# Performance work log

Measured on AMD Instinct MI355X. Metric: run time of the kernel, lower is better.

The kernel has to match this reference:

```python
import jax, jax.numpy as jnp
import numpy as np

B, S, D_MODEL, H = 2, 2048, 1024, 16
DEPTH = D_MODEL // H


def setup_inputs() -> dict:
    key = jax.random.key(0)
    ks = jax.random.split(key, 12)
    s = 1.0 / np.sqrt(D_MODEL)
    inp = {
        "q": jax.random.normal(ks[0], (B, S, D_MODEL), jnp.float32),
        "k": jax.random.normal(ks[1], (B, S, D_MODEL), jnp.float32),
        "v": jax.random.normal(ks[2], (B, S, D_MODEL), jnp.float32),
        # CTRL-style causal mask: 1 where position is disallowed (future), 0 otherwise
        "mask": jnp.triu(jnp.ones((S, S), jnp.float32), k=1),
        "Wq_w": jax.random.normal(ks[3], (D_MODEL, D_MODEL), jnp.float32) * s,
        "Wq_b": jax.random.normal(ks[4], (D_MODEL,), jnp.float32) * s,
        "Wk_w": jax.random.normal(ks[5], (D_MODEL, D_MODEL), jnp.float32) * s,
        "Wk_b": jax.random.normal(ks[6], (D_MODEL,), jnp.float32) * s,
        "Wv_w": jax.random.normal(ks[7], (D_MODEL, D_MODEL), jnp.float32) * s,
        "Wv_b": jax.random.normal(ks[8], (D_MODEL,), jnp.float32) * s,
        "dense_w": jax.random.normal(ks[9], (D_MODEL, D_MODEL), jnp.float32) * s,
        "dense_b": jax.random.normal(ks[10], (D_MODEL,), jnp.float32) * s,
    }
    return inp


def _split_heads(x):
    # [B, S, D] -> [B, H, S, depth]
    b, s, _ = x.shape
    return x.reshape(b, s, H, DEPTH).transpose(0, 2, 1, 3)


def reference(q, k, v, mask, Wq_w, Wq_b, Wk_w, Wk_b, Wv_w, Wv_b, dense_w, dense_b):
    b = q.shape[0]
    # torch Linear: y = x @ W^T + b
    qh = _split_heads(q @ Wq_w.T + Wq_b)  # [B,H,Sq,dh]
    kh = _split_heads(k @ Wk_w.T + Wk_b)  # [B,H,Sk,dh]
    vh = _split_heads(v @ Wv_w.T + Wv_b)  # [B,H,Sk,dh]

    scale = 1.0 / np.sqrt(DEPTH)
    logits = jnp.einsum("bhqd,bhkd->bhqk", qh, kh) * scale  # [B,H,Sq,Sk]
    nd, ns = logits.shape[-2], logits.shape[-1]
    logits = logits + mask[ns - nd:ns, :ns] * -10000.0
    attn = jax.nn.softmax(logits, axis=-1)
    ctx = jnp.einsum("bhqk,bhkd->bhqd", attn, vh)  # [B,H,Sq,dh]
    ctx = ctx.transpose(0, 2, 1, 3).reshape(b, -1, D_MODEL)  # [B,Sq,D]
    out = ctx @ dense_w.T + dense_b
    return out
```

## Files before the change

### kernel.cpp

```cpp
#include <hip/hip_runtime.h>
#include <hip/hip_bf16.h>

typedef __bf16 bf16x8 __attribute__((ext_vector_type(8)));
typedef __bf16 bf16x4 __attribute__((ext_vector_type(4)));
typedef float  f32x4  __attribute__((ext_vector_type(4)));

#define D_MODEL 1024
#define SEQ     2048
#define NH      16
#define DH      64
#define MTOT    4096

__device__ __forceinline__ void gload16(const void* gp, void* lp) {
  __builtin_amdgcn_global_load_lds(
      (const __attribute__((address_space(1))) unsigned int*)gp,
      (__attribute__((address_space(3))) unsigned int*)lp,
      16, 0, 0);
}

struct CvtSegs {
  const float* s[7];
  __bf16*      d[7];
  int          n8[7];
};

__global__ __launch_bounds__(256) void cvt_kernel(CvtSegs c) {
  const int seg = blockIdx.y;
  const float4* s = (const float4*)c.s[seg];
  bf16x8*       d = (bf16x8*)c.d[seg];
  const int n8 = c.n8[seg];
  for (int i = blockIdx.x * 256 + threadIdx.x; i < n8; i += gridDim.x * 256) {
    float4 a = s[2 * i];
    float4 b = s[2 * i + 1];
    bf16x8 o;
    o[0] = (__bf16)a.x; o[1] = (__bf16)a.y; o[2] = (__bf16)a.z; o[3] = (__bf16)a.w;
    o[4] = (__bf16)b.x; o[5] = (__bf16)b.y; o[6] = (__bf16)b.z; o[7] = (__bf16)b.w;
    d[i] = o;
  }
}

template <int EPI>
__device__ __forceinline__ void gemm_core(const __bf16* __restrict__ A,
                                          const __bf16* __restrict__ W,
                                          const float* __restrict__ bias,
                                          void* __restrict__ outp,
                                          __bf16* Asm, __bf16* Bsm,
                                          int row0, int col0) {
  const int tid = threadIdx.x;
  const int lane = tid & 63;
  const int w = tid >> 6;
  const int lr = lane & 15, lg = lane >> 4;
  const int wr = w >> 1, wc = w & 1;
  char* AsB = (char*)Asm;
  char* BsB = (char*)Bsm;

  f32x4 acc[4][4];
#pragma unroll
  for (int i = 0; i < 4; ++i)
#pragma unroll
    for (int j = 0; j < 4; ++j) acc[i][j] = (f32x4){0.f, 0.f, 0.f, 0.f};

  const int kch = (lane & 3) * 8;

#pragma unroll
  for (int tt = 0; tt < 2; ++tt) {
#pragma unroll
    for (int s = 0; s < 2; ++s) {
      const int cb = (w * 2 + s) * 64;
      const int arow = (cb + lane) >> 2;
      gload16(A + (size_t)(row0 + arow) * D_MODEL + tt * 32 + kch,
              AsB + tt * 8192 + cb * 16);
      gload16(W + (size_t)(col0 + arow) * D_MODEL + tt * 32 + kch,
              BsB + tt * 8192 + cb * 16);
    }
  }

  for (int t = 0; t < 32; ++t) {
    if (t < 31) asm volatile("s_waitcnt vmcnt(4)" ::: "memory");
    else        asm volatile("s_waitcnt vmcnt(0)" ::: "memory");
    __builtin_amdgcn_s_barrier();
    if (t + 2 < 32) {
      const int nb = (t + 2) % 3;
      const int k0 = (t + 2) * 32;
#pragma unroll
      for (int s = 0; s < 2; ++s) {
        const int cb = (w * 2 + s) * 64;
        const int arow = (cb + lane) >> 2;
        gload16(A + (size_t)(row0 + arow) * D_MODEL + k0 + kch,
                AsB + nb * 8192 + cb * 16);
        gload16(W + (size_t)(col0 + arow) * D_MODEL + k0 + kch,
                BsB + nb * 8192 + cb * 16);
      }
    }
    {
      char* Ab = AsB + (t % 3) * 8192;
      char* Bb = BsB + (t % 3) * 8192;
      bf16x8 af[4], bfr[4];
#pragma unroll
      for (int mi = 0; mi < 4; ++mi)
        af[mi] = *(const bf16x8*)(Ab + (wr * 64 + mi * 16 + lr) * 64 + lg * 16);
#pragma unroll
      for (int ni = 0; ni < 4; ++ni)
        bfr[ni] = *(const bf16x8*)(Bb + (wc * 64 + ni * 16 + lr) * 64 + lg * 16);
      __builtin_amdgcn_s_setprio(1);
#pragma unroll
      for (int mi = 0; mi < 4; ++mi)
#pragma unroll
        for (int ni = 0; ni < 4; ++ni)
          acc[mi][ni] = __builtin_amdgcn_mfma_f32_16x16x32_bf16(af[mi], bfr[ni],
                                                                acc[mi][ni], 0, 0, 0);
      __builtin_amdgcn_s_setprio(0);
      __builtin_amdgcn_sched_barrier(0);
    }
  }

  if (EPI == 2) {
    __bf16* o = (__bf16*)outp;
#pragma unroll
    for (int mi = 0; mi < 4; ++mi) {
#pragma unroll
      for (int ni = 0; ni < 4; ++ni) {
        const int n = col0 + wc * 64 + ni * 16 + lr;
        const float bv = bias[n];
        const int m0 = row0 + wr * 64 + mi * 16 + lg * 4;
        bf16x4 pk;
#pragma unroll
        for (int j = 0; j < 4; ++j) pk[j] = (__bf16)(acc[mi][ni][j] + bv);
        *(bf16x4*)(o + ((size_t)((m0 >> 11) * NH + (n >> 6)) * DH + (n & 63)) * SEQ +
                   (m0 & 2047)) = pk;
      }
    }
  } else {
#pragma unroll
    for (int mi = 0; mi < 4; ++mi) {
#pragma unroll
      for (int ni = 0; ni < 4; ++ni) {
        const int n = col0 + wc * 64 + ni * 16 + lr;
        const float bv = bias[n];
#pragma unroll
        for (int j = 0; j < 4; ++j) {
          const int m = row0 + wr * 64 + mi * 16 + lg * 4 + j;
          const float v = acc[mi][ni][j] + bv;
          if (EPI == 0) {
            __bf16* o = (__bf16*)outp;
            o[(size_t)((m >> 11) * NH + (n >> 6)) * (SEQ * DH) +
              (size_t)(m & 2047) * DH + (n & 63)] = (__bf16)v;
          } else {
            float* o = (float*)outp;
            o[(size_t)m * D_MODEL + n] = v;
          }
        }
      }
    }
  }
}

struct QkvPtrs {
  const __bf16* A[3];
  const __bf16* W[3];
  const float*  b[3];
  __bf16*       o[3];
};

__global__ __launch_bounds__(256, 3) void gemm_qkv_kernel(QkvPtrs p) {
  __shared__ __bf16 As[3][128 * 32];
  __shared__ __bf16 Bs[3][128 * 32];
  const int z = blockIdx.z;
  if (z == 2)
    gemm_core<2>(p.A[z], p.W[z], p.b[z], p.o[z], &As[0][0], &Bs[0][0],
                 blockIdx.x * 128, blockIdx.y * 128);
  else
    gemm_core<0>(p.A[z], p.W[z], p.b[z], p.o[z], &As[0][0], &Bs[0][0],
                 blockIdx.x * 128, blockIdx.y * 128);
}

__global__ __launch_bounds__(256, 3) void gemm_out_kernel(const __bf16* __restrict__ A,
                                                          const __bf16* __restrict__ W,
                                                          const float* __restrict__ b,
                                                          float* __restrict__ o) {
  __shared__ __bf16 As[3][128 * 32];
  __shared__ __bf16 Bs[3][128 * 32];
  gemm_core<1>(A, W, b, o, &As[0][0], &Bs[0][0], blockIdx.x * 128, blockIdx.y * 128);
}

__global__ __launch_bounds__(256, 4) void attn_kernel(const __bf16* __restrict__ qh,
                                                      const __bf16* __restrict__ kh,
                                                      const __bf16* __restrict__ vt,
                                                      __bf16* __restrict__ ctx) {
  __shared__ __bf16 Ks[2][64 * 64];
  __shared__ __bf16 Vt[2][64 * 64];
  __shared__ __bf16 Ps[4][16 * 64];

  const int bh = blockIdx.x;
  const int qb = 31 - blockIdx.y;
  const int tid = threadIdx.x, lane = tid & 63, w = tid >> 6;
  const int lr = lane & 15, lg = lane >> 4;
  const size_t hoff = (size_t)bh * SEQ * DH;
  const __bf16* Q   = qh + hoff;
  const __bf16* Kp  = kh + hoff;
  const __bf16* Vtp = vt + hoff;
  const int q0 = qb * 64 + w * 16;

  bf16x8 qf[2];
#pragma unroll
  for (int ki = 0; ki < 2; ++ki)
    qf[ki] = *(const bf16x8*)(Q + (size_t)(q0 + lr) * DH + ki * 32 + lg * 8);

  f32x4 o[4];
#pragma unroll
  for (int ni = 0; ni < 4; ++ni) o[ni] = (f32x4){0.f, 0.f, 0.f, 0.f};
  float lsum = 0.f;

  char* Psw = (char*)Ps[w];
  const int nt = qb + 1;

#pragma unroll
  for (int s = 0; s < 2; ++s) {
    const int c = (w * 2 + s) * 64 + lane;
    const int row = c >> 3;
    const int gch = (c & 7) ^ (row & 7);
    gload16(Kp + (size_t)row * DH + gch * 8, (char*)Ks[0] + (w * 2 + s) * 1024);
    gload16(Vtp + (size_t)row * SEQ + gch * 8, (char*)Vt[0] + (w * 2 + s) * 1024);
  }

  int cur = 0;
  for (int t = 0; t < nt; ++t) {
    __syncthreads();
    if (t + 1 < nt) {
      const int nxt = cur ^ 1;
#pragma unroll
      for (int s = 0; s < 2; ++s) {
        const int c = (w * 2 + s) * 64 + lane;
        const int row = c >> 3;
        const int gch = (c & 7) ^ (row & 7);
        gload16(Kp + (size_t)((t + 1) * 64 + row) * DH + gch * 8,
                (char*)Ks[nxt] + (w * 2 + s) * 1024);
        gload16(Vtp + (size_t)row * SEQ + (t + 1) * 64 + gch * 8,
                (char*)Vt[nxt] + (w * 2 + s) * 1024);
      }
    }
    {
      char* KsB = (char*)Ks[cur];
      char* VtB = (char*)Vt[cur];

      f32x4 st[4];
#pragma unroll
      for (int ni = 0; ni < 4; ++ni) st[ni] = (f32x4){0.f, 0.f, 0.f, 0.f};
      __builtin_amdgcn_s_setprio(1);
#pragma unroll
      for (int ki = 0; ki < 2; ++ki) {
        const int kc = ki * 4 + lg;
#pragma unroll
        for (int ni = 0; ni < 4; ++ni) {
          const int row = ni * 16 + lr;
          bf16x8 kf = *(const bf16x8*)(KsB + row * 128 + ((kc ^ (row & 7)) << 4));
          st[ni] = __builtin_amdgcn_mfma_f32_16x16x32_bf16(kf, qf[ki], st[ni], 0, 0, 0);
        }
      }
      __builtin_amdgcn_s_setprio(0);

      const int kvb = t * 64;
      const bool needmask = (kvb + 63 > q0);
      const int q = q0 + lr;
      float p[4][4];
      float psum = 0.f;
#pragma unroll
      for (int ni = 0; ni < 4; ++ni) {
#pragma unroll
        for (int j = 0; j < 4; ++j) {
          float v = st[ni][j] * 0.18033688f;
          if (needmask && (kvb + ni * 16 + lg * 4 + j > q)) v = -1e9f;
          const float pe = __builtin_amdgcn_exp2f(v);
          p[ni][j] = pe;
          psum += pe;
        }
      }
      lsum += psum;

#pragma unroll
      for (int ni = 0; ni < 4; ++ni) {
        bf16x4 pk;
#pragma unroll
        for (int j = 0; j < 4; ++j) pk[j] = (__bf16)p[ni][j];
        const int chunk = 2 * ni + (lg >> 1);
        *(bf16x4*)(Psw + lr * 128 + ((chunk ^ (lr & 7)) << 4) + (lg & 1) * 8) = pk;
      }
      asm volatile("s_waitcnt lgkmcnt(0)" ::: "memory");
      __builtin_amdgcn_sched_barrier(0);

      __builtin_amdgcn_s_setprio(1);
#pragma unroll
      for (int ki = 0; ki < 2; ++ki) {
        const int kc = ki * 4 + lg;
        bf16x8 pf2 = *(const bf16x8*)(Psw + lr * 128 + ((kc ^ (lr & 7)) << 4));
#pragma unroll
        for (int ni = 0; ni < 4; ++ni) {
          const int d = ni * 16 + lr;
          bf16x8 vf = *(const bf16x8*)(VtB + d * 128 + ((kc ^ (lr & 7)) << 4));
          o[ni] = __builtin_amdgcn_mfma_f32_16x16x32_bf16(pf2, vf, o[ni], 0, 0, 0);
        }
      }
      __builtin_amdgcn_s_setprio(0);
    }
    cur ^= 1;
  }

  lsum += __shfl_xor(lsum, 16, 64);
  lsum += __shfl_xor(lsum, 32, 64);
  const int bb = bh >> 4, hh = bh & 15;
#pragma unroll
  for (int j = 0; j < 4; ++j) {
    const int row = lg * 4 + j;
    const float inv = 1.0f / __shfl(lsum, row, 64);
    const int qrow = q0 + row;
    __bf16* orow = ctx + (size_t)(bb * SEQ + qrow) * D_MODEL + hh * DH;
#pragma unroll
    for (int ni = 0; ni < 4; ++ni)
      orow[ni * 16 + lr] = (__bf16)(o[ni][j] * inv);
  }
}

extern "C" void kernel_launch(void* const* d_in, const int* in_sizes, int n_in,
                              void* d_out, int out_size, void* d_ws, size_t ws_size,
                              hipStream_t stream) {
  (void)in_sizes; (void)n_in; (void)out_size; (void)ws_size;
  const float* q  = (const float*)d_in[0];
  const float* k  = (const float*)d_in[1];
  const float* v  = (const float*)d_in[2];
  const float* Wq = (const float*)d_in[4];
  const float* bq = (const float*)d_in[5];
  const float* Wk = (const float*)d_in[6];
  const float* bk = (const float*)d_in[7];
  const float* Wv = (const float*)d_in[8];
  const float* bv = (const float*)d_in[9];
  const float* Wd = (const float*)d_in[10];
  const float* bd = (const float*)d_in[11];

  char* ws = (char*)d_ws;
  __bf16* qb  = (__bf16*)(ws + 0);
  __bf16* kb  = (__bf16*)(ws + 8388608);
  __bf16* vb  = (__bf16*)(ws + 16777216);
  __bf16* wqb = (__bf16*)(ws + 25165824);
  __bf16* wkb = (__bf16*)(ws + 27262976);
  __bf16* wvb = (__bf16*)(ws + 29360128);
  __bf16* wdb = (__bf16*)(ws + 31457280);
  __bf16* qhp = (__bf16*)(ws + 33554432);
  __bf16* khp = (__bf16*)(ws + 41943040);
  __bf16* vtp = (__bf16*)(ws + 50331648);
  __bf16* ctxp= (__bf16*)(ws + 58720256);

  CvtSegs cs;
  cs.s[0] = q;  cs.d[0] = qb;  cs.n8[0] = 524288;
  cs.s[1] = k;  cs.d[1] = kb;  cs.n8[1] = 524288;
  cs.s[2] = v;  cs.d[2] = vb;  cs.n8[2] = 524288;
  cs.s[3] = Wq; cs.d[3] = wqb; cs.n8[3] = 131072;
  cs.s[4] = Wk; cs.d[4] = wkb; cs.n8[4] = 131072;
  cs.s[5] = Wv; cs.d[5] = wvb; cs.n8[5] = 131072;
  cs.s[6] = Wd; cs.d[6] = wdb; cs.n8[6] = 131072;
  cvt_kernel<<<dim3(256, 7, 1), dim3(256), 0, stream>>>(cs);

  QkvPtrs qp;
  qp.A[0] = qb;  qp.A[1] = kb;  qp.A[2] = vb;
  qp.W[0] = wqb; qp.W[1] = wkb; qp.W[2] = wvb;
  qp.b[0] = bq;  qp.b[1] = bk;  qp.b[2] = bv;
  qp.o[0] = qhp; qp.o[1] = khp; qp.o[2] = vtp;
  gemm_qkv_kernel<<<dim3(32, 8, 3), dim3(256), 0, stream>>>(qp);

  attn_kernel<<<dim3(32, 32, 1), dim3(256), 0, stream>>>(qhp, khp, vtp, ctxp);

  gemm_out_kernel<<<dim3(32, 8, 1), dim3(256), 0, stream>>>(ctxp, wdb, bd, (float*)d_out);
}
```

Baseline: 117.1 us.

## Split attention KV tiles across waves with per-wave buffers and LDS reduction

Restructures the attention kernel so that each of the four waves handles all 64 query rows, and the 32-wide KV tiles are split round-robin across waves instead of splitting query rows. Each wave keeps its own double-buffered K/V/P region in LDS and uses vmcnt waits instead of block-wide barriers in the main loop. At the end, partial outputs and row sums are reduced across waves through LDS. The aim is to remove per-iteration __syncthreads and reuse K/V fragments across four query sub-tiles. In exchange it uses 80KB of LDS, more accumulator registers and an occupancy hint lowered from 4 to 2, and adds a final cross-wave reduction.

```diff
diff --git a/kernel.cpp b/kernel.cpp
--- a/kernel.cpp
+++ b/kernel.cpp
@@ -183,13 +183,11 @@
   gemm_core<1>(A, W, b, o, &As[0][0], &Bs[0][0], blockIdx.x * 128, blockIdx.y * 128);
 }
 
-__global__ __launch_bounds__(256, 4) void attn_kernel(const __bf16* __restrict__ qh,
+__global__ __launch_bounds__(256, 2) void attn_kernel(const __bf16* __restrict__ qh,
                                                       const __bf16* __restrict__ kh,
                                                       const __bf16* __restrict__ vt,
                                                       __bf16* __restrict__ ctx) {
-  __shared__ __bf16 Ks[2][64 * 64];
-  __shared__ __bf16 Vt[2][64 * 64];
-  __shared__ __bf16 Ps[4][16 * 64];
+  __shared__ __align__(16) char LDS[81920];
 
   const int bh = blockIdx.x;
   const int qb = 31 - blockIdx.y;
@@ -199,124 +197,169 @@
   const __bf16* Q   = qh + hoff;
   const __bf16* Kp  = kh + hoff;
   const __bf16* Vtp = vt + hoff;
-  const int q0 = qb * 64 + w * 16;
-
-  bf16x8 qf[2];
-#pragma unroll
-  for (int ki = 0; ki < 2; ++ki)
-    qf[ki] = *(const bf16x8*)(Q + (size_t)(q0 + lr) * DH + ki * 32 + lg * 8);
-
-  f32x4 o[4];
-#pragma unroll
-  for (int ni = 0; ni < 4; ++ni) o[ni] = (f32x4){0.f, 0.f, 0.f, 0.f};
-  float lsum = 0.f;
-
-  char* Psw = (char*)Ps[w];
-  const int nt = qb + 1;
-
-#pragma unroll
-  for (int s = 0; s < 2; ++s) {
-    const int c = (w * 2 + s) * 64 + lane;
-    const int row = c >> 3;
-    const int gch = (c & 7) ^ (row & 7);
-    gload16(Kp + (size_t)row * DH + gch * 8, (char*)Ks[0] + (w * 2 + s) * 1024);
-    gload16(Vtp + (size_t)row * SEQ + gch * 8, (char*)Vt[0] + (w * 2 + s) * 1024);
-  }
+  const int q0 = qb * 64;
+
+  bf16x8 qf[4][2];
+#pragma unroll
+  for (int qi = 0; qi < 4; ++qi)
+#pragma unroll
+    for (int ki = 0; ki < 2; ++ki)
+      qf[qi][ki] = *(const bf16x8*)(Q + (size_t)(q0 + qi * 16 + lr) * DH +
+                                    ki * 32 + lg * 8);
+
+  f32x4 o[4][4];
+#pragma unroll
+  for (int qi = 0; qi < 4; ++qi)
+#pragma unroll
+    for (int ni = 0; ni < 4; ++ni) o[qi][ni] = (f32x4){0.f, 0.f, 0.f, 0.f};
+  float ls[4] = {0.f, 0.f, 0.f, 0.f};
+
+  char* Kl = LDS + w * 20480;
+  char* Vl = Kl + 8192;
+  char* Pl = Kl + 16384;
+
+  const int ntt = 2 * qb + 2;
+  const int cnt = (ntt - w + 3) >> 2;
+
+#define STAGE_TILE(T, B)                                                      \
+  {                                                                           \
+    _Pragma("unroll") for (int g = 0; g < 4; ++g) {                           \
+      const int c = g * 64 + lane;                                            \
+      const int kr = c >> 3, kc2 = (c & 7) ^ (kr & 7);                        \
+      gload16(Kp + (size_t)((T) * 32 + kr) * DH + kc2 * 8,                    \
+              Kl + (B) * 4096 + g * 1024);                                    \
+    }                                                                         \
+    _Pragma("unroll") for (int g = 0; g < 4; ++g) {                           \
+      const int c = g * 64 + lane;                                            \
+      const int vr = c >> 2, vc2 = (c & 3) ^ (vr & 3);                        \
+      gload16(Vtp + (size_t)vr * SEQ + (T) * 32 + vc2 * 8,                    \
+              Vl + (B) * 4096 + g * 1024);                                    \
+    }                                                                         \
+  }
+
+  if (cnt > 0) STAGE_TILE(w, 0);
 
   int cur = 0;
-  for (int t = 0; t < nt; ++t) {
-    __syncthreads();
-    if (t + 1 < nt) {
-      const int nxt = cur ^ 1;
-#pragma unroll
-      for (int s = 0; s < 2; ++s) {
-        const int c = (w * 2 + s) * 64 + lane;
-        const int row = c >> 3;
-        const int gch = (c & 7) ^ (row & 7);
-        gload16(Kp + (size_t)((t + 1) * 64 + row) * DH + gch * 8,
-                (char*)Ks[nxt] + (w * 2 + s) * 1024);
-        gload16(Vtp + (size_t)row * SEQ + (t + 1) * 64 + gch * 8,
-                (char*)Vt[nxt] + (w * 2 + s) * 1024);
+  for (int it = 0; it < cnt; ++it) {
+    const int t = w + it * 4;
+    if (it + 1 < cnt) {
+      STAGE_TILE(t + 4, cur ^ 1);
+      asm volatile("s_waitcnt vmcnt(8)" ::: "memory");
+    } else {
+      asm volatile("s_waitcnt vmcnt(0)" ::: "memory");
+    }
+    __builtin_amdgcn_sched_barrier(0);
+    char* Kb = Kl + cur * 4096;
+    char* Vb = Vl + cur * 4096;
+
+    f32x4 st[2][4];
+#pragma unroll
+    for (int ni = 0; ni < 2; ++ni)
+#pragma unroll
+      for (int qi = 0; qi < 4; ++qi) st[ni][qi] = (f32x4){0.f, 0.f, 0.f, 0.f};
+    __builtin_amdgcn_s_setprio(1);
+#pragma unroll
+    for (int ki = 0; ki < 2; ++ki) {
+#pragma unroll
+      for (int ni = 0; ni < 2; ++ni) {
+        const int kr = ni * 16 + lr;
+        bf16x8 kf = *(const bf16x8*)(Kb + kr * 128 +
+                                     (((ki * 4 + lg) ^ (kr & 7)) << 4));
+#pragma unroll
+        for (int qi = 0; qi < 4; ++qi)
+          st[ni][qi] = __builtin_amdgcn_mfma_f32_16x16x32_bf16(kf, qf[qi][ki],
+                                                               st[ni][qi], 0, 0, 0);
       }
     }
-    {
-      char* KsB = (char*)Ks[cur];
-      char* VtB = (char*)Vt[cur];
-
-      f32x4 st[4];
-#pragma unroll
-      for (int ni = 0; ni < 4; ++ni) st[ni] = (f32x4){0.f, 0.f, 0.f, 0.f};
-      __builtin_amdgcn_s_setprio(1);
-#pragma unroll
-      for (int ki = 0; ki < 2; ++ki) {
-        const int kc = ki * 4 + lg;
-#pragma unroll
-        for (int ni = 0; ni < 4; ++ni) {
-          const int row = ni * 16 + lr;
-          bf16x8 kf = *(const bf16x8*)(KsB + row * 128 + ((kc ^ (row & 7)) << 4));
-          st[ni] = __builtin_amdgcn_mfma_f32_16x16x32_bf16(kf, qf[ki], st[ni], 0, 0, 0);
+    __builtin_amdgcn_s_setprio(0);
+
+    const int kvb = t * 32;
+    const bool needmask = (kvb + 31 > q0);
+#pragma unroll
+    for (int ni = 0; ni < 2; ++ni) {
+#pragma unroll
+      for (int qi = 0; qi < 4; ++qi) {
+        bf16x4 pk;
+#pragma unroll
+        for (int j = 0; j < 4; ++j) {
+          float v = st[ni][qi][j] * 0.18033688f;
+          if (needmask && (kvb + ni * 16 + lg * 4 + j > q0 + qi * 16 + lr))
+            v = -1e9f;
+          const float pe = __builtin_amdgcn_exp2f(v);
+          ls[qi] += pe;
+          pk[j] = (__bf16)pe;
         }
+        const int q = qi * 16 + lr;
+        const int ch = (ni * 2 + (lg >> 1)) ^ (q & 3);
+        *(bf16x4*)(Pl + q * 64 + ch * 16 + (lg & 1) * 8) = pk;
       }
-      __builtin_amdgcn_s_setprio(0);
-
-      const int kvb = t * 64;
-      const bool needmask = (kvb + 63 > q0);
-      const int q = q0 + lr;
-      float p[4][4];
-      float psum = 0.f;
-#pragma unroll
-      for (int ni = 0; ni < 4; ++ni) {
-#pragma unroll
-        for (int j = 0; j < 4; ++j) {
-          float v = st[ni][j] * 0.18033688f;
-          if (needmask && (kvb + ni * 16 + lg * 4 + j > q)) v = -1e9f;
-          const float pe = __builtin_amdgcn_exp2f(v);
-          p[ni][j] = pe;
-          psum += pe;
-        }
-      }
-      lsum += psum;
-
-#pragma unroll
-      for (int ni = 0; ni < 4; ++ni) {
-        bf16x4 pk;
-#pragma unroll
-        for (int j = 0; j < 4; ++j) pk[j] = (__bf16)p[ni][j];
-        const int chunk = 2 * ni + (lg >> 1);
-        *(bf16x4*)(Psw + lr * 128 + ((chunk ^ (lr & 7)) << 4) + (lg & 1) * 8) = pk;
-      }
-      asm volatile("s_waitcnt lgkmcnt(0)" ::: "memory");
-      __builtin_amdgcn_sched_barrier(0);
-
-      __builtin_amdgcn_s_setprio(1);
-#pragma unroll
-      for (int ki = 0; ki < 2; ++ki) {
-        const int kc = ki * 4 + lg;
-        bf16x8 pf2 = *(const bf16x8*)(Psw + lr * 128 + ((kc ^ (lr & 7)) << 4));
-#pragma unroll
-        for (int ni = 0; ni < 4; ++ni) {
-          const int d = ni * 16 + lr;
-          bf16x8 vf = *(const bf16x8*)(VtB + d * 128 + ((kc ^ (lr & 7)) << 4));
-          o[ni] = __builtin_amdgcn_mfma_f32_16x16x32_bf16(pf2, vf, o[ni], 0, 0, 0);
-        }
-      }
-      __builtin_amdgcn_s_setprio(0);
-    }
+    }
+    asm volatile("s_waitcnt lgkmcnt(0)" ::: "memory");
+    __builtin_amdgcn_sched_barrier(0);
+
+    bf16x8 pf[4], vf[4];
+#pragma unroll
+    for (int qi = 0; qi < 4; ++qi) {
+      const int q = qi * 16 + lr;
+      pf[qi] = *(const bf16x8*)(Pl + q * 64 + ((lg ^ (q & 3)) << 4));
+    }
+#pragma unroll
+    for (int ni = 0; ni < 4; ++ni) {
+      const int d = ni * 16 + lr;
+      vf[ni] = *(const bf16x8*)(Vb + d * 64 + ((lg ^ (d & 3)) << 4));
+    }
+    __builtin_amdgcn_s_setprio(1);
+#pragma unroll
+    for (int qi = 0; qi < 4; ++qi)
+#pragma unroll
+      for (int ni = 0; ni < 4; ++ni)
+        o[qi][ni] = __builtin_amdgcn_mfma_f32_16x16x32_bf16(pf[qi], vf[ni],
+                                                            o[qi][ni], 0, 0, 0);
+    __builtin_amdgcn_s_setprio(0);
     cur ^= 1;
   }
-
-  lsum += __shfl_xor(lsum, 16, 64);
-  lsum += __shfl_xor(lsum, 32, 64);
+#undef STAGE_TILE
+
+  __syncthreads();
+  float* Op = (float*)LDS + w * 4352;
+#pragma unroll
+  for (int qi = 0; qi < 4; ++qi)
+#pragma unroll
+    for (int ni = 0; ni < 4; ++ni)
+      *(f32x4*)(Op + (ni * 16 + lr) * 68 + qi * 16 + lg * 4) = o[qi][ni];
+  {
+    float* Lp = (float*)LDS + 17408 + (w * 4 + lg) * 64;
+#pragma unroll
+    for (int qi = 0; qi < 4; ++qi) Lp[qi * 16 + lr] = ls[qi];
+  }
+  __syncthreads();
+
+  f32x4 a2[4];
+#pragma unroll
+  for (int r = 0; r < 4; ++r) a2[r] = (f32x4){0.f, 0.f, 0.f, 0.f};
+#pragma unroll
+  for (int p = 0; p < 4; ++p) {
+    const float* Pp = (const float*)LDS + p * 4352;
+#pragma unroll
+    for (int r = 0; r < 4; ++r)
+      a2[r] += *(const f32x4*)(Pp + (r * 16 + lr) * 68 + w * 16 + lg * 4);
+  }
+  float Lt = 0.f;
+#pragma unroll
+  for (int k = 0; k < 4; ++k)
+    Lt += ((const float*)LDS)[17408 + (k * 4 + lg) * 64 + w * 16 + lr];
+  Lt += __shfl_xor(Lt, 16, 64);
+  Lt += __shfl_xor(Lt, 32, 64);
+
   const int bb = bh >> 4, hh = bh & 15;
 #pragma unroll
   for (int j = 0; j < 4; ++j) {
-    const int row = lg * 4 + j;
-    const float inv = 1.0f / __shfl(lsum, row, 64);
-    const int qrow = q0 + row;
+    const float inv = 1.0f / __shfl(Lt, lg * 4 + j, 16);
+    const int qrow = q0 + w * 16 + lg * 4 + j;
     __bf16* orow = ctx + (size_t)(bb * SEQ + qrow) * D_MODEL + hh * DH;
 #pragma unroll
-    for (int ni = 0; ni < 4; ++ni)
-      orow[ni * 16 + lr] = (__bf16)(o[ni][j] * inv);
+    for (int r = 0; r < 4; ++r)
+      orow[r * 16 + lr] = (__bf16)(a2[r][j] * inv);
   }
 }
 
```

Result: no change. 114.9 us (-1.9%).
